# Performance work log

Measured on AMD Instinct MI355X. Metric: run time of the kernel, lower is better.

## Reference

```python
import jax, jax.numpy as jnp
import numpy as np

V, C, DFF, NH, NL, KS, OUT = 256, 192, 768, 2, 6, 3, 192
B, T, W = 64, 512, 4
DH = C // NH
PAD = KS // 2
DN = ('NCH', 'OIH', 'NCH')


def _rel_to_abs(x):
    # [b,h,l,2l-1] -> [b,h,l,l]  (VITS _relative_position_to_absolute_position)
    b, h, l, _ = x.shape
    x = jnp.pad(x, ((0, 0), (0, 0), (0, 0), (0, 1)))
    x = x.reshape(b, h, l * 2 * l)
    x = jnp.pad(x, ((0, 0), (0, 0), (0, l - 1)))
    x = x.reshape(b, h, l + 1, 2 * l - 1)
    return x[:, :, :l, l - 1:]


def _abs_to_rel(x):
    # [b,h,l,l] -> [b,h,l,2l-1]  (VITS _absolute_position_to_relative_position)
    b, h, l, _ = x.shape
    x = jnp.pad(x, ((0, 0), (0, 0), (0, 0), (0, l - 1)))
    x = x.reshape(b, h, l * (2 * l - 1))
    x = jnp.pad(x, ((0, 0), (0, 0), (l, 0)))
    x = x.reshape(b, h, l, 2 * l)
    return x[:, :, :, 1:]


def _get_rel_emb(emb, length):
    # emb: [2W+1, DH] -> [2*length-1, DH]
    pad_len = max(length - (W + 1), 0)
    start = max(W + 1 - length, 0)
    padded = jnp.pad(emb, ((pad_len, pad_len), (0, 0)))
    return padded[start:start + 2 * length - 1]


def _ln(x, g, b):
    mu = jnp.mean(x, -1, keepdims=True)
    var = jnp.mean(jnp.square(x - mu), -1, keepdims=True)
    return (x - mu) * jax.lax.rsqrt(var + 1e-5) * g + b


def setup_inputs():
    key = jax.random.key(0)
    ks = jax.random.split(key, 12)
    n = lambda k, s, std: jax.random.normal(k, s, jnp.float32) * std
    return dict(
        tokens=jax.random.randint(ks[0], (B, T), 0, V),
        x_lengths=jnp.full((B,), T, dtype=jnp.int32),
        emb_w=n(ks[1], (V, C), C ** -0.5),
        wqkv=n(ks[2], (NL, 3, C, C), 0.02),
        bqkv=jnp.zeros((NL, 3, C), jnp.float32),
        wo=n(ks[3], (NL, C, C), 0.02),
        bo=jnp.zeros((NL, C), jnp.float32),
        rel_k=n(ks[4], (NL, 2 * W + 1, DH), DH ** -0.5),
        rel_v=n(ks[5], (NL, 2 * W + 1, DH), DH ** -0.5),
        ln1_g=jnp.ones((NL, C), jnp.float32),
        ln1_b=jnp.zeros((NL, C), jnp.float32),
        ln2_g=jnp.ones((NL, C), jnp.float32),
        ln2_b=jnp.zeros((NL, C), jnp.float32),
        ffn_w1=n(ks[6], (NL, DFF, C, KS), 0.02),
        ffn_b1=jnp.zeros((NL, DFF), jnp.float32),
        ffn_w2=n(ks[7], (NL, C, DFF, KS), 0.02),
        ffn_b2=jnp.zeros((NL, C), jnp.float32),
        proj_w=n(ks[8], (2 * OUT, C), 0.02),
        proj_b=jnp.zeros((2 * OUT,), jnp.float32),
    )


def reference(tokens, x_lengths, emb_w, wqkv, bqkv, wo, bo, rel_k, rel_v,
              ln1_g, ln1_b, ln2_g, ln2_b, ffn_w1, ffn_b1, ffn_w2, ffn_b2,
              proj_w, proj_b):
    x = emb_w[tokens] * (C ** 0.5)                       # [B,T,C]
    mask = (jnp.arange(T)[None, :] < x_lengths[:, None]).astype(x.dtype)  # [B,T]
    bias = jnp.where((mask[:, None, :, None] * mask[:, None, None, :]) > 0.0, 0.0, -1e4)
    x = x * mask[..., None]
    inv_sqrt_d = DH ** -0.5
    for l in range(NL):
        q = jnp.einsum('btc,oc->bto', x, wqkv[l, 0]) + bqkv[l, 0]
        k = jnp.einsum('btc,oc->bto', x, wqkv[l, 1]) + bqkv[l, 1]
        v = jnp.einsum('btc,oc->bto', x, wqkv[l, 2]) + bqkv[l, 2]
        q = q.reshape(B, T, NH, DH).transpose(0, 2, 1, 3)  # [B,H,T,D]
        k = k.reshape(B, T, NH, DH).transpose(0, 2, 1, 3)
        v = v.reshape(B, T, NH, DH).transpose(0, 2, 1, 3)
        scores = jnp.einsum('bhtd,bhsd->bhts', q, k) * inv_sqrt_d
        rk = _get_rel_emb(rel_k[l], T)                     # [2T-1, D]
        rel_logits = jnp.einsum('bhtd,md->bhtm', q * inv_sqrt_d, rk)
        scores = scores + _rel_to_abs(rel_logits)
        p = jax.nn.softmax(scores + bias, axis=-1)
        o = jnp.einsum('bhts,bhsd->bhtd', p, v)
        o = o + jnp.einsum('bhtm,md->bhtd', _abs_to_rel(p), _get_rel_emb(rel_v[l], T))
        o = o.transpose(0, 2, 1, 3).reshape(B, T, C)
        y = jnp.einsum('btc,oc->bto', o, wo[l]) + bo[l]
        x = _ln(x + y, ln1_g[l], ln1_b[l])
        h = jax.lax.conv_general_dilated((x * mask[..., None]).transpose(0, 2, 1),
                                         ffn_w1[l], (1,), [(PAD, PAD)],
                                         dimension_numbers=DN) + ffn_b1[l][None, :, None]
        h = jax.nn.relu(h) * mask[:, None, :]
        h = jax.lax.conv_general_dilated(h, ffn_w2[l], (1,), [(PAD, PAD)],
                                         dimension_numbers=DN) + ffn_b2[l][None, :, None]
        y = h.transpose(0, 2, 1) * mask[..., None]
        x = _ln(x + y, ln2_g[l], ln2_b[l])
    x = x * mask[..., None]
    stats = (jnp.einsum('btc,oc->bto', x, proj_w) + proj_b) * mask[..., None]
    m, logs = jnp.split(stats, 2, axis=-1)
    x_mask = mask[:, None, :]
    return x.transpose(0, 2, 1), m.transpose(0, 2, 1), logs.transpose(0, 2, 1), x_mask
```

## Files before the change

kernel.cpp:

```cpp
#include <hip/hip_runtime.h>
#include <hip/hip_bf16.h>

typedef __hip_bfloat16 bf16;
typedef __attribute__((ext_vector_type(8))) short short8;
typedef __attribute__((ext_vector_type(4))) float f32x4;

#define NB 64
#define NT 512
#define NC 192
#define NHEAD 2
#define NDH 96
#define NLAYER 6
#define NDFF 768
#define NW 4

constexpr int MROWS = NB * NT;
constexpr size_t MC = (size_t)MROWS * NC;
constexpr size_t MCB = MC * 4;
constexpr float QSC = 0.10206207261596575f * 1.4426950408889634f;

__device__ __forceinline__ float us2f(unsigned short x) { return __uint_as_float((unsigned)x << 16); }
__device__ __forceinline__ unsigned short f2b(float f) {
    bf16 h = __float2bfloat16(f);
    return *reinterpret_cast<unsigned short*>(&h);
}

__global__ __launch_bounds__(256) void cvt_frag_plain(const float* __restrict__ s, bf16* __restrict__ d,
                                                      int L, int N, int K) {
    int i = blockIdx.x * 256 + threadIdx.x;
    int total = L * (N / 16) * (K / 32) * 64;
    if (i >= total) return;
    int lane = i & 63;
    int tile = i >> 6;
    int nbk = K / 32;
    int kb = tile % nbk;
    int rest = tile / nbk;
    int nb = rest % (N / 16);
    int l = rest / (N / 16);
    int li = lane & 15, g = lane >> 4;
    const float* src = s + ((size_t)l * N + nb * 16 + li) * K + kb * 32 + g * 8;
    bf16* dst = d + (size_t)i * 8;
#pragma unroll
    for (int u = 0; u < 8; u++) dst[u] = __float2bfloat16(src[u]);
}
__global__ __launch_bounds__(256) void cvt_frag_conv(const float* __restrict__ s, bf16* __restrict__ d,
                                                     int L, int N, int C) {
    int i = blockIdx.x * 256 + threadIdx.x;
    int total = L * 3 * (N / 16) * (C / 32) * 64;
    if (i >= total) return;
    int lane = i & 63;
    int tile = i >> 6;
    int nbk = C / 32;
    int kb = tile % nbk;
    int rest = tile / nbk;
    int nb = rest % (N / 16);
    int rest2 = rest / (N / 16);
    int dk = rest2 % 3;
    int l = rest2 / 3;
    int li = lane & 15, g = lane >> 4;
    const float* src = s + (((size_t)l * N + nb * 16 + li) * C + kb * 32 + g * 8) * 3 + dk;
    bf16* dst = d + (size_t)i * 8;
#pragma unroll
    for (int u = 0; u < 8; u++) dst[u] = __float2bfloat16(src[u * 3]);
}

__global__ __launch_bounds__(256) void embed_kernel(const int* __restrict__ tok,
                                                    const int* __restrict__ lens,
                                                    const float* __restrict__ emb,
                                                    bf16* __restrict__ xb) {
    int idx = blockIdx.x * 256 + threadIdx.x;
    if (idx >= (int)MC) return;
    int c = idx % NC;
    int m = idx / NC;
    int t = m % NT, b = m / NT;
    float v = emb[tok[m] * NC + c] * 13.856406460551018f;
    if (t >= lens[b]) v = 0.f;
    xb[idx] = __float2bfloat16(v);
}

enum GMode { GM_QKV = 0, GM_CONV1 = 2, GM_PROJ = 4 };

template <int MODE, int NTOT, int KC, int TAPS, int BN>
__global__ __launch_bounds__(256) void gemm_mfma(const bf16* __restrict__ A,
                                                 const bf16* __restrict__ W,
                                                 const float* __restrict__ bias,
                                                 const int* __restrict__ lens,
                                                 float* __restrict__ of,
                                                 bf16* __restrict__ ob1,
                                                 bf16* __restrict__ ob2,
                                                 bf16* __restrict__ ob3) {
    constexpr int RA = (TAPS == 3) ? 130 : 128;
    constexpr int NBN = NTOT / 16;
    constexpr int NBK = KC / 32;
    constexpr int NSUB = BN / 16;
    __shared__ unsigned short As[RA * 40];
    const int tid = threadIdx.x;
    const int w = tid >> 6, lane = tid & 63;
    const int g = lane >> 4, li = lane & 15;
    const int n0 = blockIdx.x * BN;
    const int m0 = blockIdx.y * 128;
    const int b = m0 >> 9, t0 = m0 & 511;
    const int len = lens[b];
    const int nbBase = n0 >> 4;
    const unsigned short* Au = (const unsigned short*)A;
    const unsigned short* Wu = (const unsigned short*)W;

    f32x4 acc[2][NSUB];
#pragma unroll
    for (int a = 0; a < 2; a++)
#pragma unroll
        for (int s = 0; s < NSUB; s++) acc[a][s] = (f32x4){0.f, 0.f, 0.f, 0.f};

#pragma unroll 1
    for (int k0 = 0; k0 < KC; k0 += 32) {
        const int kb = k0 >> 5;
        __syncthreads();
        for (int c = tid; c < RA * 2; c += 256) {
            int i = c >> 1, hf = (c & 1) * 16;
            int t = t0 + i - (TAPS == 3 ? 1 : 0);
            bool valid = (t >= 0) && (t < NT);
            if constexpr (MODE == GM_CONV1) valid = valid && (t < len);
            short8 v0{}, v1{};
            if (valid) {
                const unsigned short* src = Au + ((size_t)(b * NT + t) * KC + k0 + hf);
                v0 = *(const short8*)src;
                v1 = *(const short8*)(src + 8);
            }
            *(short8*)&As[i * 40 + hf] = v0;
            *(short8*)&As[i * 40 + hf + 8] = v1;
        }
        __syncthreads();
#pragma unroll
        for (int dk = 0; dk < TAPS; dk++) {
            short8 af0 = *(const short8*)&As[(w * 32 + li + dk) * 40 + g * 8];
            short8 af1 = *(const short8*)&As[(w * 32 + 16 + li + dk) * 40 + g * 8];
#pragma unroll
            for (int sub = 0; sub < NSUB; sub++) {
                short8 bfr = *(const short8*)(Wu +
                    ((((size_t)(dk * NBN + nbBase + sub)) * NBK + kb) << 9) + (lane << 3));
                acc[0][sub] = __builtin_amdgcn_mfma_f32_16x16x32_bf16(af0, bfr, acc[0][sub], 0, 0, 0);
                acc[1][sub] = __builtin_amdgcn_mfma_f32_16x16x32_bf16(af1, bfr, acc[1][sub], 0, 0, 0);
            }
        }
    }

#pragma unroll
    for (int sub = 0; sub < NSUB; sub++) {
        int n = n0 + sub * 16 + li;
        float bv = bias[n];
#pragma unroll
        for (int a = 0; a < 2; a++) {
#pragma unroll
            for (int rr = 0; rr < 4; rr++) {
                int t = t0 + w * 32 + a * 16 + g * 4 + rr;
                size_t m = (size_t)(b * NT + t);
                float vv = acc[a][sub][rr] + bv;
                if constexpr (MODE == GM_QKV) {
                    int iw = n / NC;
                    int cc = n - iw * NC;
                    int hh = cc >= NDH ? 1 : 0;
                    int d = cc - hh * NDH;
                    int bh = b * NHEAD + hh;
                    if (iw == 0) ob1[((size_t)bh * NT + t) * NDH + d] = __float2bfloat16(vv * QSC);
                    else if (iw == 1) ob2[((size_t)bh * NT + t) * NDH + d] = __float2bfloat16(vv);
                    else ob3[((size_t)bh * NDH + d) * NT + t] = __float2bfloat16(vv);
                } else if constexpr (MODE == GM_CONV1) {
                    vv = vv > 0.f ? vv : 0.f;
                    if (t >= len) vv = 0.f;
                    ob1[m * NDFF + n] = __float2bfloat16(vv);
                } else {
                    if (t >= len) vv = 0.f;
                    int half = n >= 192 ? 1 : 0;
                    int cc = n - half * 192;
                    of[(size_t)(half + 1) * MC + ((size_t)b * NC + cc) * NT + t] = vv;
                }
            }
        }
    }
}

template <int KC, int TAPS, bool MASKY, int BM, bool FINAL>
__global__ __launch_bounds__(512, 4) void gemm_ln(const bf16* __restrict__ A,
                                                  const bf16* __restrict__ W,
                                                  const float* __restrict__ bias,
                                                  const int* __restrict__ lens,
                                                  const float* __restrict__ lng,
                                                  const float* __restrict__ lnb,
                                                  bf16* __restrict__ xb,
                                                  float* __restrict__ of) {
    constexpr int RA = BM + ((TAPS == 3) ? 2 : 0);
    constexpr int NSTEP = KC / 32;
    constexpr int NBN = 12;
    constexpr int NBK = KC / 32;
    constexpr int AR = BM / 32;
    __shared__ unsigned short As[RA * 40];
    __shared__ float rsm[BM][4];
    __shared__ float rsq[BM][4];
    const int tid = threadIdx.x;
    const int lane = tid & 63;
    const int g = lane >> 4, li = lane & 15;
    const int w = tid >> 6;
    const int wr = w & 1, wc = w >> 1;
    const int m0 = blockIdx.x * BM;
    const int b = m0 >> 9, t0 = m0 & 511;
    const int len = lens[b];
    const unsigned short* Au = (const unsigned short*)A;
    const unsigned short* Wu = (const unsigned short*)W;
    unsigned short* Xu = (unsigned short*)xb;

    const int ai = tid >> 1, ahf = (tid & 1) * 16;
    const int at = t0 + ai - (TAPS == 3 ? 1 : 0);
    const bool aon = (tid < RA * 2);
    const bool avalid = aon && (at >= 0) && (at < NT);

    short8 ra0{}, ra1{};
    short8 bcur[TAPS][3], bnxt[TAPS][3];

    f32x4 acc[AR][3];
#pragma unroll
    for (int ar = 0; ar < AR; ar++)
#pragma unroll
        for (int sub = 0; sub < 3; sub++) acc[ar][sub] = (f32x4){0.f, 0.f, 0.f, 0.f};

    if (avalid) {
        const unsigned short* src = Au + ((size_t)(b * NT + at) * KC + 0 + ahf);
        ra0 = *(const short8*)src;
        ra1 = *(const short8*)(src + 8);
    }
#pragma unroll
    for (int dk = 0; dk < TAPS; dk++)
#pragma unroll
        for (int sub = 0; sub < 3; sub++)
            bcur[dk][sub] = *(const short8*)(Wu +
                ((((size_t)(dk * NBN + wc * 3 + sub)) * NBK) << 9) + (lane << 3));
    if (aon) {
        short8 z{};
        *(short8*)&As[ai * 40 + ahf] = avalid ? ra0 : z;
        *(short8*)&As[ai * 40 + ahf + 8] = avalid ? ra1 : z;
    }

#pragma unroll 1
    for (int s = 0; s < NSTEP; s++) {
        __syncthreads();
        if (s + 1 < NSTEP) {
            int k0 = (s + 1) * 32;
            if (avalid) {
                const unsigned short* src = Au + ((size_t)(b * NT + at) * KC + k0 + ahf);
                ra0 = *(const short8*)src;
                ra1 = *(const short8*)(src + 8);
            }
#pragma unroll
            for (int dk = 0; dk < TAPS; dk++)
#pragma unroll
                for (int sub = 0; sub < 3; sub++)
                    bnxt[dk][sub] = *(const short8*)(Wu +
                        ((((size_t)(dk * NBN + wc * 3 + sub)) * NBK + (s + 1)) << 9) + (lane << 3));
        }
#pragma unroll
        for (int dk = 0; dk < TAPS; dk++) {
            short8 af[AR];
#pragma unroll
            for (int ar = 0; ar < AR; ar++)
                af[ar] = *(const short8*)&As[(wr * (BM / 2) + ar * 16 + li + dk) * 40 + g * 8];
#pragma unroll
            for (int sub = 0; sub < 3; sub++) {
#pragma unroll
                for (int ar = 0; ar < AR; ar++)
                    acc[ar][sub] = __builtin_amdgcn_mfma_f32_16x16x32_bf16(af[ar], bcur[dk][sub], acc[ar][sub], 0, 0, 0);
            }
        }
        __syncthreads();
        if (s + 1 < NSTEP) {
            if (aon) {
                short8 z{};
                *(short8*)&As[ai * 40 + ahf] = avalid ? ra0 : z;
                *(short8*)&As[ai * 40 + ahf + 8] = avalid ? ra1 : z;
            }
#pragma unroll
            for (int dk = 0; dk < TAPS; dk++)
#pragma unroll
                for (int sub = 0; sub < 3; sub++) bcur[dk][sub] = bnxt[dk][sub];
        }
    }

    float biasv[3], gv[3], bbv[3];
#pragma unroll
    for (int sub = 0; sub < 3; sub++) {
        int n = wc * 48 + sub * 16 + li;
        biasv[sub] = bias[n];
        gv[sub] = lng[n];
        bbv[sub] = lnb[n];
    }
    float psm[AR][4], psq[AR][4];
#pragma unroll
    for (int ar = 0; ar < AR; ar++) {
#pragma unroll
        for (int rr = 0; rr < 4; rr++) {
            int r = wr * (BM / 2) + ar * 16 + 4 * g + rr;
            int t = t0 + r;
            size_t m = (size_t)(b * NT + t);
            float sm = 0.f, sq = 0.f;
#pragma unroll
            for (int sub = 0; sub < 3; sub++) {
                int n = wc * 48 + sub * 16 + li;
                float y = acc[ar][sub][rr] + biasv[sub];
                if (MASKY && t >= len) y = 0.f;
                float rres = y + us2f(Xu[m * NC + n]);
                acc[ar][sub][rr] = rres;
                sm += rres;
                sq += rres * rres;
            }
            psm[ar][rr] = sm;
            psq[ar][rr] = sq;
        }
    }
#pragma unroll
    for (int off = 1; off < 16; off <<= 1) {
#pragma unroll
        for (int ar = 0; ar < AR; ar++)
#pragma unroll
            for (int rr = 0; rr < 4; rr++) {
                psm[ar][rr] += __shfl_xor(psm[ar][rr], off);
                psq[ar][rr] += __shfl_xor(psq[ar][rr], off);
            }
    }
    if (li == 0) {
#pragma unroll
        for (int ar = 0; ar < AR; ar++)
#pragma unroll
            for (int rr = 0; rr < 4; rr++) {
                int r = wr * (BM / 2) + ar * 16 + 4 * g + rr;
                rsm[r][wc] = psm[ar][rr];
                rsq[r][wc] = psq[ar][rr];
            }
    }
    __syncthreads();
#pragma unroll
    for (int ar = 0; ar < AR; ar++) {
#pragma unroll
        for (int rr = 0; rr < 4; rr++) {
            int r = wr * (BM / 2) + ar * 16 + 4 * g + rr;
            int t = t0 + r;
            size_t m = (size_t)(b * NT + t);
            float sm = rsm[r][0] + rsm[r][1] + rsm[r][2] + rsm[r][3];
            float sq = rsq[r][0] + rsq[r][1] + rsq[r][2] + rsq[r][3];
            float mu = sm * (1.f / NC);
            float var = fmaxf(sq * (1.f / NC) - mu * mu, 0.f);
            float rs = rsqrtf(var + 1e-5f);
#pragma unroll
            for (int sub = 0; sub < 3; sub++) {
                int n = wc * 48 + sub * 16 + li;
                float o = (acc[ar][sub][rr] - mu) * rs * gv[sub] + bbv[sub];
                Xu[m * NC + n] = f2b(o);
                if (FINAL) of[((size_t)b * NC + n) * NT + t] = (t < len) ? o : 0.f;
            }
        }
    }
}

__global__ __launch_bounds__(256, 4) void attn_mfma(const bf16* __restrict__ q,
                                                    const bf16* __restrict__ k,
                                                    const bf16* __restrict__ v,
                                                    const float* __restrict__ relk,
                                                    const float* __restrict__ relv,
                                                    const int* __restrict__ lens,
                                                    bf16* __restrict__ o) {
    __shared__ __align__(16) char pool[40448];
    unsigned short* Kt = (unsigned short*)pool;
    unsigned short* Vt = (unsigned short*)(pool + 13312);
    unsigned short* Pt = (unsigned short*)(pool + 27136);
    unsigned short* Pb = (unsigned short*)(pool + 36352);
    unsigned short* Qt = (unsigned short*)pool;
    unsigned short* Rk = (unsigned short*)(pool + 13312);

    const int bh = blockIdx.x, qt = blockIdx.y;
    const int b = bh >> 1, h = bh & 1;
    const int q0 = qt * 64;
    const int tid = threadIdx.x;
    const int w = tid >> 6, lane = tid & 63;
    const int g = lane >> 4, li = lane & 15;
    const int len = lens[b];
    const bool anymask = (len < NT);

    const unsigned short* qg = (const unsigned short*)q + (size_t)bh * NT * NDH;
    const unsigned short* kg = (const unsigned short*)k + (size_t)bh * NT * NDH;
    const unsigned short* vg = (const unsigned short*)v + (size_t)bh * NDH * NT;

    for (int c = tid; c < 64 * 12; c += 256) {
        int r = c / 12, seg = (c % 12) * 8;
        *(short8*)&Qt[r * 104 + seg] = *(const short8*)(qg + (size_t)(q0 + r) * NDH + seg);
    }
    for (int c = tid; c < 16 * 96; c += 256) {
        int dd = c / 96, d = c - (c / 96) * 96;
        Rk[dd * 104 + d] = (dd < 9) ? f2b(relk[dd * 96 + d]) : (unsigned short)0;
    }
    for (int c = tid; c < 4 * 16 * 32; c += 256) Pb[c] = 0;
    __syncthreads();

    f32x4 racc = (f32x4){0.f, 0.f, 0.f, 0.f};
    short8 qf[3];
#pragma unroll
    for (int kk = 0; kk < 3; kk++) {
        qf[kk] = *(const short8*)&Qt[(w * 16 + li) * 104 + kk * 32 + g * 8];
        short8 bfr = *(const short8*)&Rk[li * 104 + kk * 32 + g * 8];
        racc = __builtin_amdgcn_mfma_f32_16x16x32_bf16(qf[kk], bfr, racc, 0, 0, 0);
    }
    short8 rvf[6];
#pragma unroll
    for (int ds = 0; ds < 6; ds++) {
#pragma unroll
        for (int i = 0; i < 8; i++) {
            int j = g * 8 + i;
            int d = ds * 16 + li;
            unsigned short u = (j < 9) ? f2b(relv[j * 96 + d]) : (unsigned short)0;
            rvf[ds][i] = (short)u;
        }
    }
    short8 bones;
#pragma unroll
    for (int i = 0; i < 8; i++) bones[i] = (li == 0) ? (short)0x3F80 : (short)0;
    __syncthreads();

    float m_run[4];
    f32x4 Oa[7];
#pragma unroll
    for (int rr = 0; rr < 4; rr++) m_run[rr] = -1e30f;
#pragma unroll
    for (int ds = 0; ds < 7; ds++) Oa[ds] = (f32x4){0.f, 0.f, 0.f, 0.f};

    const int wrow0 = q0 + w * 16;

    for (int s0 = 0; s0 < NT; s0 += 64) {
        for (int c = tid; c < 64 * 12; c += 256) {
            int ss = c / 12, seg = (c % 12) * 8;
            *(short8*)&Kt[ss * 104 + seg] = *(const short8*)(kg + (size_t)(s0 + ss) * NDH + seg);
        }
        for (int c = tid; c < 96 * 8; c += 256) {
            int d = c >> 3, seg = (c & 7) * 8;
            *(short8*)&Vt[d * 72 + seg] = *(const short8*)(vg + (size_t)d * NT + s0 + seg);
        }
        __syncthreads();

        const bool band = (s0 <= wrow0 + 15 + NW) && (s0 + 63 >= wrow0 - NW);

        f32x4 acc[4];
#pragma unroll
        for (int sub = 0; sub < 4; sub++) acc[sub] = (f32x4){0.f, 0.f, 0.f, 0.f};
        __builtin_amdgcn_s_setprio(1);
#pragma unroll
        for (int kk = 0; kk < 3; kk++) {
#pragma unroll
            for (int sub = 0; sub < 4; sub++) {
                short8 bfr = *(const short8*)&Kt[(sub * 16 + li) * 104 + kk * 32 + g * 8];
                acc[sub] = __builtin_amdgcn_mfma_f32_16x16x32_bf16(qf[kk], bfr, acc[sub], 0, 0, 0);
            }
        }
        __builtin_amdgcn_s_setprio(0);

        if (band) {
#pragma unroll
            for (int sub = 0; sub < 4; sub++) {
#pragma unroll
                for (int rr = 0; rr < 4; rr++) {
                    int scol = s0 + sub * 16 + li;
                    int qrow = wrow0 + 4 * g + rr;
                    int dd = scol - qrow;
                    float rv = __shfl(racc[rr], g * 16 + dd + NW);
                    if (dd >= -NW && dd <= NW) acc[sub][rr] += rv;
                }
            }
        }
        if (anymask) {
#pragma unroll
            for (int sub = 0; sub < 4; sub++) {
#pragma unroll
                for (int rr = 0; rr < 4; rr++) {
                    int scol = s0 + sub * 16 + li;
                    int qrow = wrow0 + 4 * g + rr;
                    if (scol >= len || qrow >= len) acc[sub][rr] -= 14427.0f;
                }
            }
        }
        float pmr[4];
#pragma unroll
        for (int rr = 0; rr < 4; rr++) {
            pmr[rr] = fmaxf(fmaxf(acc[0][rr], acc[1][rr]), fmaxf(acc[2][rr], acc[3][rr]));
        }
        float growth = fmaxf(fmaxf(pmr[0] - m_run[0], pmr[1] - m_run[1]),
                             fmaxf(pmr[2] - m_run[2], pmr[3] - m_run[3]));
        if (__any(growth > 11.54f)) {
#pragma unroll
            for (int off = 1; off < 16; off <<= 1)
#pragma unroll
                for (int rr = 0; rr < 4; rr++) pmr[rr] = fmaxf(pmr[rr], __shfl_xor(pmr[rr], off));
#pragma unroll
            for (int rr = 0; rr < 4; rr++) {
                float mn = fmaxf(m_run[rr], pmr[rr]);
                float scf = exp2f(m_run[rr] - mn);
                m_run[rr] = mn;
#pragma unroll
                for (int ds = 0; ds < 7; ds++) Oa[ds][rr] *= scf;
            }
        }
#pragma unroll
        for (int sub = 0; sub < 4; sub++)
#pragma unroll
            for (int rr = 0; rr < 4; rr++)
                acc[sub][rr] = exp2f(acc[sub][rr] - m_run[rr]);

#pragma unroll
        for (int sub = 0; sub < 4; sub++)
#pragma unroll
            for (int rr = 0; rr < 4; rr++)
                Pt[w * 1152 + (4 * g + rr) * 72 + sub * 16 + li] = f2b(acc[sub][rr]);

        __builtin_amdgcn_s_setprio(1);
#pragma unroll
        for (int kk = 0; kk < 2; kk++) {
            short8 pa = *(const short8*)&Pt[w * 1152 + li * 72 + kk * 32 + g * 8];
#pragma unroll
            for (int ds = 0; ds < 6; ds++) {
                short8 bv = *(const short8*)&Vt[(ds * 16 + li) * 72 + kk * 32 + g * 8];
                Oa[ds] = __builtin_amdgcn_mfma_f32_16x16x32_bf16(pa, bv, Oa[ds], 0, 0, 0);
            }
            Oa[6] = __builtin_amdgcn_mfma_f32_16x16x32_bf16(pa, bones, Oa[6], 0, 0, 0);
        }
        __builtin_amdgcn_s_setprio(0);

        if (band) {
            for (int j = g; j < 9; j += 4) {
                int u = wrow0 + li + j - NW - s0;
                unsigned short pv_ = (u >= 0 && u < 64) ? Pt[w * 1152 + li * 72 + u] : (unsigned short)0;
                Pb[w * 512 + li * 32 + j] = pv_;
            }
            short8 pband = *(const short8*)&Pb[w * 512 + li * 32 + g * 8];
#pragma unroll
            for (int ds = 0; ds < 6; ds++)
                Oa[ds] = __builtin_amdgcn_mfma_f32_16x16x32_bf16(pband, rvf[ds], Oa[ds], 0, 0, 0);
        }
        __syncthreads();
    }

    float invl[4];
#pragma unroll
    for (int rr = 0; rr < 4; rr++) invl[rr] = 1.f / __shfl(Oa[6][rr], lane & 48);
#pragma unroll
    for (int ds = 0; ds < 6; ds++)
#pragma unroll
        for (int rr = 0; rr < 4; rr++) {
            int qrow = wrow0 + 4 * g + rr;
            o[((size_t)(b * NT + qrow)) * NC + h * 96 + ds * 16 + li] =
                __float2bfloat16(Oa[ds][rr] * invl[rr]);
        }
}

__global__ __launch_bounds__(256) void mask_kernel(const int* __restrict__ lens, float* __restrict__ out) {
    int idx = blockIdx.x * 256 + threadIdx.x;
    if (idx >= NB * NT) return;
    int t = idx % NT;
    int b = idx / NT;
    out[idx] = (t < lens[b]) ? 1.f : 0.f;
}

extern "C" void kernel_launch(void* const* d_in, const int* in_sizes, int n_in,
                              void* d_out, int out_size, void* d_ws, size_t ws_size,
                              hipStream_t stream) {
    (void)in_sizes; (void)n_in; (void)out_size; (void)ws_size;
    const int* tok = (const int*)d_in[0];
    const int* lens = (const int*)d_in[1];
    const float* emb = (const float*)d_in[2];
    const float* wqkv = (const float*)d_in[3];
    const float* bqkv = (const float*)d_in[4];
    const float* wo = (const float*)d_in[5];
    const float* bo = (const float*)d_in[6];
    const float* relk = (const float*)d_in[7];
    const float* relv = (const float*)d_in[8];
    const float* ln1g = (const float*)d_in[9];
    const float* ln1b = (const float*)d_in[10];
    const float* ln2g = (const float*)d_in[11];
    const float* ln2b = (const float*)d_in[12];
    const float* fw1 = (const float*)d_in[13];
    const float* fb1 = (const float*)d_in[14];
    const float* fw2 = (const float*)d_in[15];
    const float* fb2 = (const float*)d_in[16];
    const float* pw = (const float*)d_in[17];
    const float* pb = (const float*)d_in[18];
    float* out = (float*)d_out;

    char* wsb = (char*)d_ws;
    bf16* xb = (bf16*)(wsb + 2 * MCB);
    bf16* qb = (bf16*)(wsb + 2 * MCB + MCB / 2);
    bf16* kb = qb + MC;
    bf16* vb = kb + MC;
    bf16* ob = vb + MC;
    bf16* hB = qb;
    bf16* pwqkv = ob + MC;
    bf16* pwo = pwqkv + (size_t)NLAYER * 3 * NC * NC;
    bf16* pw1 = pwo + (size_t)NLAYER * NC * NC;
    bf16* pw2 = pw1 + (size_t)NLAYER * 3 * NDFF * NC;
    bf16* pproj = pw2 + (size_t)NLAYER * 3 * NC * NDFF;

    {
        int n1 = NLAYER * 36 * 6 * 64;
        cvt_frag_plain<<<(n1 + 255) / 256, 256, 0, stream>>>(wqkv, pwqkv, NLAYER, 576, 192);
        int n2 = NLAYER * 12 * 6 * 64;
        cvt_frag_plain<<<(n2 + 255) / 256, 256, 0, stream>>>(wo, pwo, NLAYER, 192, 192);
        int n3 = 1 * 24 * 6 * 64;
        cvt_frag_plain<<<(n3 + 255) / 256, 256, 0, stream>>>(pw, pproj, 1, 384, 192);
        int n4 = NLAYER * 3 * 48 * 6 * 64;
        cvt_frag_conv<<<(n4 + 255) / 256, 256, 0, stream>>>(fw1, pw1, NLAYER, 768, 192);
        int n5 = NLAYER * 3 * 12 * 24 * 64;
        cvt_frag_conv<<<(n5 + 255) / 256, 256, 0, stream>>>(fw2, pw2, NLAYER, 192, 768);
    }

    embed_kernel<<<(int)((MC + 255) / 256), 256, 0, stream>>>(tok, lens, emb, xb);

    for (int l = 0; l < NLAYER; l++) {
        gemm_mfma<GM_QKV, 576, 192, 1, 64><<<dim3(9, 256), 256, 0, stream>>>(
            xb, pwqkv + (size_t)l * 3 * NC * NC, bqkv + (size_t)l * 3 * NC, lens,
            nullptr, qb, kb, vb);
        attn_mfma<<<dim3(NB * NHEAD, 8), 256, 0, stream>>>(
            qb, kb, vb, relk + (size_t)l * (2 * NW + 1) * NDH,
            relv + (size_t)l * (2 * NW + 1) * NDH, lens, ob);
        gemm_ln<192, 1, false, 64, false><<<512, 512, 0, stream>>>(
            ob, pwo + (size_t)l * NC * NC, bo + (size_t)l * NC, lens,
            ln1g + (size_t)l * NC, ln1b + (size_t)l * NC, xb, nullptr);
        gemm_mfma<GM_CONV1, 768, 192, 3, 64><<<dim3(12, 256), 256, 0, stream>>>(
            xb, pw1 + (size_t)l * 3 * NDFF * NC, fb1 + (size_t)l * NDFF, lens,
            nullptr, hB, nullptr, nullptr);
        if (l < NLAYER - 1) {
            gemm_ln<768, 3, true, 64, false><<<512, 512, 0, stream>>>(
                hB, pw2 + (size_t)l * 3 * NC * NDFF, fb2 + (size_t)l * NC, lens,
                ln2g + (size_t)l * NC, ln2b + (size_t)l * NC, xb, nullptr);
        } else {
            gemm_ln<768, 3, true, 64, true><<<512, 512, 0, stream>>>(
                hB, pw2 + (size_t)l * 3 * NC * NDFF, fb2 + (size_t)l * NC, lens,
                ln2g + (size_t)l * NC, ln2b + (size_t)l * NC, xb, out);
        }
    }

    gemm_mfma<GM_PROJ, 384, 192, 1, 64><<<dim3(6, 256), 256, 0, stream>>>(
        xb, pproj, pb, lens, out, nullptr, nullptr, nullptr);
    mask_kernel<<<(NB * NT + 255) / 256, 256, 0, stream>>>(lens, out + 3 * MC);
}
```

Baseline: 1.348 ms.

## Retile QKV/conv1 GEMMs with register prefetch and double-buffer attention K/V loads

```diff
diff --git a/kernel.cpp b/kernel.cpp
--- a/kernel.cpp
+++ b/kernel.cpp
@@ -78,26 +78,155 @@
     xb[idx] = __float2bfloat16(v);
 }
 
-enum GMode { GM_QKV = 0, GM_CONV1 = 2, GM_PROJ = 4 };
-
-template <int MODE, int NTOT, int KC, int TAPS, int BN>
-__global__ __launch_bounds__(256) void gemm_mfma(const bf16* __restrict__ A,
+#define FM_QKV 0
+#define FM_CONV1 1
+
+template <int FMODE, int NTOT, int KC, int TAPS>
+__global__ __launch_bounds__(512, 4) void gemm_fused(const bf16* __restrict__ A,
+                                                     const bf16* __restrict__ W,
+                                                     const float* __restrict__ bias,
+                                                     const int* __restrict__ lens,
+                                                     bf16* __restrict__ ob1,
+                                                     bf16* __restrict__ ob2,
+                                                     bf16* __restrict__ ob3) {
+    constexpr int RA = 64 + ((TAPS == 3) ? 2 : 0);
+    constexpr int NSTEP = KC / 32;
+    constexpr int NBN = NTOT / 16;
+    constexpr int NBK = KC / 32;
+    __shared__ unsigned short As[RA * 40];
+    const int tid = threadIdx.x;
+    const int lane = tid & 63;
+    const int g = lane >> 4, li = lane & 15;
+    const int w = tid >> 6;
+    const int wr = w & 1, wc = w >> 1;
+    const int n0 = blockIdx.x * 192;
+    const int m0 = blockIdx.y * 64;
+    const int b = m0 >> 9, t0 = m0 & 511;
+    const int len = lens[b];
+    const unsigned short* Au = (const unsigned short*)A;
+    const unsigned short* Wu = (const unsigned short*)W;
+
+    const int ai = tid >> 1, ahf = (tid & 1) * 16;
+    const int at = t0 + ai - (TAPS == 3 ? 1 : 0);
+    const bool aon = (tid < RA * 2);
+    bool av = aon && (at >= 0) && (at < NT);
+    if constexpr (FMODE == FM_CONV1) av = av && (at < len);
+    const bool avalid = av;
+
+    short8 ra0{}, ra1{};
+    short8 bcur[TAPS][3], bnxt[TAPS][3];
+
+    f32x4 acc[2][3];
+#pragma unroll
+    for (int ar = 0; ar < 2; ar++)
+#pragma unroll
+        for (int sub = 0; sub < 3; sub++) acc[ar][sub] = (f32x4){0.f, 0.f, 0.f, 0.f};
+
+    if (avalid) {
+        const unsigned short* src = Au + ((size_t)(b * NT + at) * KC + 0 + ahf);
+        ra0 = *(const short8*)src;
+        ra1 = *(const short8*)(src + 8);
+    }
+#pragma unroll
+    for (int dk = 0; dk < TAPS; dk++)
+#pragma unroll
+        for (int sub = 0; sub < 3; sub++) {
+            int nb = (n0 >> 4) + wc * 3 + sub;
+            bcur[dk][sub] = *(const short8*)(Wu +
+                ((((size_t)(dk * NBN + nb)) * NBK) << 9) + (lane << 3));
+        }
+    if (aon) {
+        short8 z{};
+        *(short8*)&As[ai * 40 + ahf] = avalid ? ra0 : z;
+        *(short8*)&As[ai * 40 + ahf + 8] = avalid ? ra1 : z;
+    }
+
+#pragma unroll 1
+    for (int s = 0; s < NSTEP; s++) {
+        __syncthreads();
+        if (s + 1 < NSTEP) {
+            int k0 = (s + 1) * 32;
+            if (avalid) {
+                const unsigned short* src = Au + ((size_t)(b * NT + at) * KC + k0 + ahf);
+                ra0 = *(const short8*)src;
+                ra1 = *(const short8*)(src + 8);
+            }
+#pragma unroll
+            for (int dk = 0; dk < TAPS; dk++)
+#pragma unroll
+                for (int sub = 0; sub < 3; sub++) {
+                    int nb = (n0 >> 4) + wc * 3 + sub;
+                    bnxt[dk][sub] = *(const short8*)(Wu +
+                        ((((size_t)(dk * NBN + nb)) * NBK + (s + 1)) << 9) + (lane << 3));
+                }
+        }
+#pragma unroll
+        for (int dk = 0; dk < TAPS; dk++) {
+            short8 af0 = *(const short8*)&As[(wr * 32 + li + dk) * 40 + g * 8];
+            short8 af1 = *(const short8*)&As[(wr * 32 + 16 + li + dk) * 40 + g * 8];
+#pragma unroll
+            for (int sub = 0; sub < 3; sub++) {
+                acc[0][sub] = __builtin_amdgcn_mfma_f32_16x16x32_bf16(af0, bcur[dk][sub], acc[0][sub], 0, 0, 0);
+                acc[1][sub] = __builtin_amdgcn_mfma_f32_16x16x32_bf16(af1, bcur[dk][sub], acc[1][sub], 0, 0, 0);
+            }
+        }
+        __syncthreads();
+        if (s + 1 < NSTEP) {
+            if (aon) {
+                short8 z{};
+                *(short8*)&As[ai * 40 + ahf] = avalid ? ra0 : z;
+                *(short8*)&As[ai * 40 + ahf + 8] = avalid ? ra1 : z;
+            }
+#pragma unroll
+            for (int dk = 0; dk < TAPS; dk++)
+#pragma unroll
+                for (int sub = 0; sub < 3; sub++) bcur[dk][sub] = bnxt[dk][sub];
+        }
+    }
+
+#pragma unroll
+    for (int sub = 0; sub < 3; sub++) {
+        int n = n0 + wc * 48 + sub * 16 + li;
+        float bv = bias[n];
+#pragma unroll
+        for (int ar = 0; ar < 2; ar++) {
+#pragma unroll
+            for (int rr = 0; rr < 4; rr++) {
+                int t = t0 + wr * 32 + ar * 16 + 4 * g + rr;
+                size_t m = (size_t)(b * NT + t);
+                float vv = acc[ar][sub][rr] + bv;
+                if constexpr (FMODE == FM_QKV) {
+                    int iw = blockIdx.x;
+                    int cc = wc * 48 + sub * 16 + li;
+                    int hh = cc >= NDH ? 1 : 0;
+                    int d = cc - hh * NDH;
+                    int bh = b * NHEAD + hh;
+                    if (iw == 0) ob1[((size_t)bh * NT + t) * NDH + d] = __float2bfloat16(vv * QSC);
+                    else if (iw == 1) ob2[((size_t)bh * NT + t) * NDH + d] = __float2bfloat16(vv);
+                    else ob3[((size_t)bh * NDH + d) * NT + t] = __float2bfloat16(vv);
+                } else {
+                    vv = vv > 0.f ? vv : 0.f;
+                    if (t >= len) vv = 0.f;
+                    ob1[m * NDFF + n] = __float2bfloat16(vv);
+                }
+            }
+        }
+    }
+}
+
+template <int NTOT, int KC>
+__global__ __launch_bounds__(256) void gemm_proj(const bf16* __restrict__ A,
                                                  const bf16* __restrict__ W,
                                                  const float* __restrict__ bias,
                                                  const int* __restrict__ lens,
-                                                 float* __restrict__ of,
-                                                 bf16* __restrict__ ob1,
-                                                 bf16* __restrict__ ob2,
-                                                 bf16* __restrict__ ob3) {
-    constexpr int RA = (TAPS == 3) ? 130 : 128;
+                                                 float* __restrict__ of) {
     constexpr int NBN = NTOT / 16;
     constexpr int NBK = KC / 32;
-    constexpr int NSUB = BN / 16;
-    __shared__ unsigned short As[RA * 40];
+    __shared__ unsigned short As[128 * 40];
     const int tid = threadIdx.x;
     const int w = tid >> 6, lane = tid & 63;
     const int g = lane >> 4, li = lane & 15;
-    const int n0 = blockIdx.x * BN;
+    const int n0 = blockIdx.x * 64;
     const int m0 = blockIdx.y * 128;
     const int b = m0 >> 9, t0 = m0 & 511;
     const int len = lens[b];
@@ -105,47 +234,37 @@
     const unsigned short* Au = (const unsigned short*)A;
     const unsigned short* Wu = (const unsigned short*)W;
 
-    f32x4 acc[2][NSUB];
+    f32x4 acc[2][4];
 #pragma unroll
     for (int a = 0; a < 2; a++)
 #pragma unroll
-        for (int s = 0; s < NSUB; s++) acc[a][s] = (f32x4){0.f, 0.f, 0.f, 0.f};
+        for (int s = 0; s < 4; s++) acc[a][s] = (f32x4){0.f, 0.f, 0.f, 0.f};
 
 #pragma unroll 1
     for (int k0 = 0; k0 < KC; k0 += 32) {
         const int kb = k0 >> 5;
         __syncthreads();
-        for (int c = tid; c < RA * 2; c += 256) {
+        for (int c = tid; c < 128 * 2; c += 256) {
             int i = c >> 1, hf = (c & 1) * 16;
-            int t = t0 + i - (TAPS == 3 ? 1 : 0);
-            bool valid = (t >= 0) && (t < NT);
-            if constexpr (MODE == GM_CONV1) valid = valid && (t < len);
-            short8 v0{}, v1{};
-            if (valid) {
-                const unsigned short* src = Au + ((size_t)(b * NT + t) * KC + k0 + hf);
-                v0 = *(const short8*)src;
-                v1 = *(const short8*)(src + 8);
-            }
-            *(short8*)&As[i * 40 + hf] = v0;
-            *(short8*)&As[i * 40 + hf + 8] = v1;
+            int t = t0 + i;
+            const unsigned short* src = Au + ((size_t)(b * NT + t) * KC + k0 + hf);
+            *(short8*)&As[i * 40 + hf] = *(const short8*)src;
+            *(short8*)&As[i * 40 + hf + 8] = *(const short8*)(src + 8);
         }
         __syncthreads();
-#pragma unroll
-        for (int dk = 0; dk < TAPS; dk++) {
-            short8 af0 = *(const short8*)&As[(w * 32 + li + dk) * 40 + g * 8];
-            short8 af1 = *(const short8*)&As[(w * 32 + 16 + li + dk) * 40 + g * 8];
-#pragma unroll
-            for (int sub = 0; sub < NSUB; sub++) {
-                short8 bfr = *(const short8*)(Wu +
-                    ((((size_t)(dk * NBN + nbBase + sub)) * NBK + kb) << 9) + (lane << 3));
-                acc[0][sub] = __builtin_amdgcn_mfma_f32_16x16x32_bf16(af0, bfr, acc[0][sub], 0, 0, 0);
-                acc[1][sub] = __builtin_amdgcn_mfma_f32_16x16x32_bf16(af1, bfr, acc[1][sub], 0, 0, 0);
-            }
-        }
-    }
-
-#pragma unroll
-    for (int sub = 0; sub < NSUB; sub++) {
+        short8 af0 = *(const short8*)&As[(w * 32 + li) * 40 + g * 8];
+        short8 af1 = *(const short8*)&As[(w * 32 + 16 + li) * 40 + g * 8];
+#pragma unroll
+        for (int sub = 0; sub < 4; sub++) {
+            short8 bfr = *(const short8*)(Wu +
+                ((((size_t)(nbBase + sub)) * NBK + kb) << 9) + (lane << 3));
+            acc[0][sub] = __builtin_amdgcn_mfma_f32_16x16x32_bf16(af0, bfr, acc[0][sub], 0, 0, 0);
+            acc[1][sub] = __builtin_amdgcn_mfma_f32_16x16x32_bf16(af1, bfr, acc[1][sub], 0, 0, 0);
+        }
+    }
+
+#pragma unroll
+    for (int sub = 0; sub < 4; sub++) {
         int n = n0 + sub * 16 + li;
         float bv = bias[n];
 #pragma unroll
@@ -153,27 +272,11 @@
 #pragma unroll
             for (int rr = 0; rr < 4; rr++) {
                 int t = t0 + w * 32 + a * 16 + g * 4 + rr;
-                size_t m = (size_t)(b * NT + t);
                 float vv = acc[a][sub][rr] + bv;
-                if constexpr (MODE == GM_QKV) {
-                    int iw = n / NC;
-                    int cc = n - iw * NC;
-                    int hh = cc >= NDH ? 1 : 0;
-                    int d = cc - hh * NDH;
-                    int bh = b * NHEAD + hh;
-                    if (iw == 0) ob1[((size_t)bh * NT + t) * NDH + d] = __float2bfloat16(vv * QSC);
-                    else if (iw == 1) ob2[((size_t)bh * NT + t) * NDH + d] = __float2bfloat16(vv);
-                    else ob3[((size_t)bh * NDH + d) * NT + t] = __float2bfloat16(vv);
-                } else if constexpr (MODE == GM_CONV1) {
-                    vv = vv > 0.f ? vv : 0.f;
-                    if (t >= len) vv = 0.f;
-                    ob1[m * NDFF + n] = __float2bfloat16(vv);
-                } else {
-                    if (t >= len) vv = 0.f;
-                    int half = n >= 192 ? 1 : 0;
-                    int cc = n - half * 192;
-                    of[(size_t)(half + 1) * MC + ((size_t)b * NC + cc) * NT + t] = vv;
-                }
+                if (t >= len) vv = 0.f;
+                int half = n >= 192 ? 1 : 0;
+                int cc = n - half * 192;
+                of[(size_t)(half + 1) * MC + ((size_t)b * NC + cc) * NT + t] = vv;
             }
         }
     }
@@ -386,6 +489,14 @@
     const unsigned short* kg = (const unsigned short*)k + (size_t)bh * NT * NDH;
     const unsigned short* vg = (const unsigned short*)v + (size_t)bh * NDH * NT;
 
+    const int kR0 = tid / 12, kS0 = (tid % 12) * 8;
+    const int kR1 = (tid + 256) / 12, kS1 = ((tid + 256) % 12) * 8;
+    const int kR2 = (tid + 512) / 12, kS2 = ((tid + 512) % 12) * 8;
+    const int vD0 = tid >> 3, vS0 = (tid & 7) * 8;
+    const int vD1 = (tid + 256) >> 3, vS1 = ((tid + 256) & 7) * 8;
+    const int vD2 = (tid + 512) >> 3, vS2 = ((tid + 512) & 7) * 8;
+    short8 k0r{}, k1r{}, k2r{}, v0r{}, v1r{}, v2r{};
+
     for (int c = tid; c < 64 * 12; c += 256) {
         int r = c / 12, seg = (c % 12) * 8;
         *(short8*)&Qt[r * 104 + seg] = *(const short8*)(qg + (size_t)(q0 + r) * NDH + seg);
@@ -396,6 +507,13 @@
     }
     for (int c = tid; c < 4 * 16 * 32; c += 256) Pb[c] = 0;
     __syncthreads();
+
+    k0r = *(const short8*)(kg + (size_t)kR0 * NDH + kS0);
+    k1r = *(const short8*)(kg + (size_t)kR1 * NDH + kS1);
+    k2r = *(const short8*)(kg + (size_t)kR2 * NDH + kS2);
+    v0r = *(const short8*)(vg + (size_t)vD0 * NT + 0 + vS0);
+    v1r = *(const short8*)(vg + (size_t)vD1 * NT + 0 + vS1);
+    v2r = *(const short8*)(vg + (size_t)vD2 * NT + 0 + vS2);
 
     f32x4 racc = (f32x4){0.f, 0.f, 0.f, 0.f};
     short8 qf[3];
@@ -420,6 +538,12 @@
 #pragma unroll
     for (int i = 0; i < 8; i++) bones[i] = (li == 0) ? (short)0x3F80 : (short)0;
     __syncthreads();
+    *(short8*)&Kt[kR0 * 104 + kS0] = k0r;
+    *(short8*)&Kt[kR1 * 104 + kS1] = k1r;
+    *(short8*)&Kt[kR2 * 104 + kS2] = k2r;
+    *(short8*)&Vt[vD0 * 72 + vS0] = v0r;
+    *(short8*)&Vt[vD1 * 72 + vS1] = v1r;
+    *(short8*)&Vt[vD2 * 72 + vS2] = v2r;
 
     float m_run[4];
     f32x4 Oa[7];
@@ -431,15 +555,16 @@
     const int wrow0 = q0 + w * 16;
 
     for (int s0 = 0; s0 < NT; s0 += 64) {
-        for (int c = tid; c < 64 * 12; c += 256) {
-            int ss = c / 12, seg = (c % 12) * 8;
-            *(short8*)&Kt[ss * 104 + seg] = *(const short8*)(kg + (size_t)(s0 + ss) * NDH + seg);
-        }
-        for (int c = tid; c < 96 * 8; c += 256) {
-            int d = c >> 3, seg = (c & 7) * 8;
-            *(short8*)&Vt[d * 72 + seg] = *(const short8*)(vg + (size_t)d * NT + s0 + seg);
-        }
         __syncthreads();
+        if (s0 + 64 < NT) {
+            int sn = s0 + 64;
+            k0r = *(const short8*)(kg + (size_t)(sn + kR0) * NDH + kS0);
+            k1r = *(const short8*)(kg + (size_t)(sn + kR1) * NDH + kS1);
+            k2r = *(const short8*)(kg + (size_t)(sn + kR2) * NDH + kS2);
+            v0r = *(const short8*)(vg + (size_t)vD0 * NT + sn + vS0);
+            v1r = *(const short8*)(vg + (size_t)vD1 * NT + sn + vS1);
+            v2r = *(const short8*)(vg + (size_t)vD2 * NT + sn + vS2);
+        }
 
         const bool band = (s0 <= wrow0 + 15 + NW) && (s0 + 63 >= wrow0 - NW);
 
@@ -539,6 +664,14 @@
                 Oa[ds] = __builtin_amdgcn_mfma_f32_16x16x32_bf16(pband, rvf[ds], Oa[ds], 0, 0, 0);
         }
         __syncthreads();
+        if (s0 + 64 < NT) {
+            *(short8*)&Kt[kR0 * 104 + kS0] = k0r;
+            *(short8*)&Kt[kR1 * 104 + kS1] = k1r;
+            *(short8*)&Kt[kR2 * 104 + kS2] = k2r;
+            *(short8*)&Vt[vD0 * 72 + vS0] = v0r;
+            *(short8*)&Vt[vD1 * 72 + vS1] = v1r;
+            *(short8*)&Vt[vD2 * 72 + vS2] = v2r;
+        }
     }
 
     float invl[4];
@@ -616,18 +749,18 @@
     embed_kernel<<<(int)((MC + 255) / 256), 256, 0, stream>>>(tok, lens, emb, xb);
 
     for (int l = 0; l < NLAYER; l++) {
-        gemm_mfma<GM_QKV, 576, 192, 1, 64><<<dim3(9, 256), 256, 0, stream>>>(
+        gemm_fused<FM_QKV, 576, 192, 1><<<dim3(3, 512), 512, 0, stream>>>(
             xb, pwqkv + (size_t)l * 3 * NC * NC, bqkv + (size_t)l * 3 * NC, lens,
-            nullptr, qb, kb, vb);
+            qb, kb, vb);
         attn_mfma<<<dim3(NB * NHEAD, 8), 256, 0, stream>>>(
             qb, kb, vb, relk + (size_t)l * (2 * NW + 1) * NDH,
             relv + (size_t)l * (2 * NW + 1) * NDH, lens, ob);
         gemm_ln<192, 1, false, 64, false><<<512, 512, 0, stream>>>(
             ob, pwo + (size_t)l * NC * NC, bo + (size_t)l * NC, lens,
             ln1g + (size_t)l * NC, ln1b + (size_t)l * NC, xb, nullptr);
-        gemm_mfma<GM_CONV1, 768, 192, 3, 64><<<dim3(12, 256), 256, 0, stream>>>(
+        gemm_fused<FM_CONV1, 768, 192, 3><<<dim3(4, 512), 512, 0, stream>>>(
             xb, pw1 + (size_t)l * 3 * NDFF * NC, fb1 + (size_t)l * NDFF, lens,
-            nullptr, hB, nullptr, nullptr);
+            hB, nullptr, nullptr);
         if (l < NLAYER - 1) {
             gemm_ln<768, 3, true, 64, false><<<512, 512, 0, stream>>>(
                 hB, pw2 + (size_t)l * 3 * NC * NDFF, fb2 + (size_t)l * NC, lens,
@@ -639,7 +772,7 @@
         }
     }
 
-    gemm_mfma<GM_PROJ, 384, 192, 1, 64><<<dim3(6, 256), 256, 0, stream>>>(
-        xb, pproj, pb, lens, out, nullptr, nullptr, nullptr);
+    gemm_proj<384, 192><<<dim3(6, 256), 256, 0, stream>>>(
+        xb, pproj, pb, lens, out);
     mask_kernel<<<(NB * NT + 255) / 256, 256, 0, stream>>>(lens, out + 3 * MC);
 }
```

After: 1.610 ms. +19.4%, slower.
